# Kernel tuning notes

Hardware: AMD Instinct MI355X
Metric: run time of the kernel (lower is better)

The kernel has to match this reference:

```python
import jax, jax.numpy as jnp
import numpy as np

G, N, D_IN, H = 512, 128, 128, 256  # graphs, nodes/graph, input feat, hidden


def setup_inputs() -> dict:
    key = jax.random.key(0)
    ks = jax.random.split(key, 12)
    node_features = jax.random.normal(ks[0], (G, N, D_IN), dtype=jnp.float32)
    # sparse-ish symmetric binary adjacency with self-loops (avg degree ~ 6)
    a = (jax.random.uniform(ks[1], (G, N, N)) < 0.05).astype(jnp.float32)
    adj = jnp.clip(a + jnp.swapaxes(a, 1, 2) + jnp.eye(N, dtype=jnp.float32)[None], 0.0, 1.0)
    s = 0.02
    W1 = jax.random.normal(ks[2], (D_IN, H), dtype=jnp.float32) * s
    b1 = jnp.zeros((H,), dtype=jnp.float32)
    W2 = jax.random.normal(ks[3], (H, H), dtype=jnp.float32) * s
    b2 = jnp.zeros((H,), dtype=jnp.float32)
    W3 = jax.random.normal(ks[4], (H, H), dtype=jnp.float32) * s
    b3 = jnp.zeros((H,), dtype=jnp.float32)
    Wh = jax.random.normal(ks[5], (H, 1), dtype=jnp.float32) * s
    bh = jnp.zeros((1,), dtype=jnp.float32)
    return {"node_features": node_features, "adj": adj, "W1": W1, "b1": b1,
            "W2": W2, "b2": b2, "W3": W3, "b3": b3, "Wh": Wh, "bh": bh}


def _gcn_layer(x, adj, W, b):
    # x: [G,N,d], adj: [G,N,N] -> relu(adj @ x @ W + b)
    agg = jnp.einsum('gij,gjd->gid', adj, x)
    return jax.nn.relu(jnp.einsum('gid,dh->gih', agg, W) + b)


def reference(node_features, adj, W1, b1, W2, b2, W3, b3, Wh, bh):
    x = node_features
    # per-layer conv; dropout is identity at inference (training=False)
    x = _gcn_layer(x, adj, W1, b1)
    x = _gcn_layer(x, adj, W2, b2)
    x = _gcn_layer(x, adj, W3, b3)
    pooled = jnp.mean(x, axis=1)               # [G, H] mean readout
    yhat = pooled @ Wh + bh                    # [G, 1] linear head
    return jnp.squeeze(yhat, axis=-1)          # [G]
```

## Files before the change

### kernel.cpp

```cpp
#include <hip/hip_runtime.h>
#include <hip/hip_bf16.h>

typedef __attribute__((ext_vector_type(8))) short bf16x8;
typedef __attribute__((ext_vector_type(4))) float f32x4;

#define PX 136
#define PA 136
#define PW 72
#define PG 72

static __device__ __forceinline__ unsigned short f2b(float f) {
  union { __hip_bfloat16 h; unsigned short u; } cv;
  cv.h = __float2bfloat16(f);
  return cv.u;
}

__global__ void __launch_bounds__(256) gnn_prep(const float* __restrict__ W1,
                                                const float* __restrict__ W2,
                                                const float* __restrict__ W3,
                                                unsigned short* __restrict__ wt) {
  int idx = blockIdx.x * 256 + threadIdx.x;
  unsigned short* wt1 = wt;
  unsigned short* wt2 = wt + 32768;
  unsigned short* wt3 = wt + 98304;
  if (idx < 32768) {
    int d = idx >> 8, h = idx & 255;
    wt1[h * 128 + d] = f2b(W1[idx]);
  }
  {
    int d = idx >> 8, h = idx & 255;
    wt2[h * 256 + d] = f2b(W2[idx]);
    wt3[h * 256 + d] = f2b(W3[idx]);
  }
}

__global__ void __launch_bounds__(512, 2) gnn_main(
    const float* __restrict__ xin, const float* __restrict__ adjg,
    const float* __restrict__ b1, const float* __restrict__ b2,
    const float* __restrict__ b3, const float* __restrict__ Wh,
    const float* __restrict__ bh, const unsigned short* __restrict__ wt,
    float* __restrict__ out) {
  __shared__ unsigned short sXT[256 * PX];
  __shared__ unsigned short sAdj[128 * PA];
  __shared__ unsigned short sW[256 * PW];
  __shared__ unsigned short sAggC[128 * PG];

  const int g = blockIdx.x;
  const int tid = threadIdx.x;
  const int lane = tid & 63;
  const int w = tid >> 6;
  const int l15 = lane & 15;
  const int l4 = lane >> 4;
  const int wm = w & 1;
  const int wn = w >> 1;

  const float* x0 = xin + (size_t)g * (128 * 128);
  const float* ag = adjg + (size_t)g * (128 * 128);

  {
    int row = tid >> 2;
    int c0 = (tid & 3) << 5;
    const float4* asrc = (const float4*)(ag + row * 128 + c0);
    const float4* xsrc = (const float4*)(x0 + row * 128 + c0);
#pragma unroll
    for (int q = 0; q < 8; ++q) {
      float4 v = asrc[q];
      ushort4 p;
      p.x = f2b(v.x); p.y = f2b(v.y); p.z = f2b(v.z); p.w = f2b(v.w);
      *(ushort4*)&sAdj[row * PA + c0 + q * 4] = p;
    }
#pragma unroll
    for (int q = 0; q < 8; ++q) {
      float4 v = xsrc[q];
      int d = c0 + q * 4;
      sXT[(d + 0) * PX + row] = f2b(v.x);
      sXT[(d + 1) * PX + row] = f2b(v.y);
      sXT[(d + 2) * PX + row] = f2b(v.z);
      sXT[(d + 3) * PX + row] = f2b(v.w);
    }
  }
  __syncthreads();

  f32x4 accB[4][4];

  for (int l = 0; l < 3; ++l) {
    const int Din = (l == 0) ? 128 : 256;
    const int nck = Din >> 6;
    const unsigned short* wtl = (l == 0) ? wt : (l == 1) ? wt + 32768 : wt + 98304;
    const float* bl = (l == 0) ? b1 : (l == 1) ? b2 : b3;

#pragma unroll
    for (int mi = 0; mi < 4; ++mi)
#pragma unroll
      for (int ni = 0; ni < 4; ++ni)
        accB[mi][ni] = (f32x4){0.f, 0.f, 0.f, 0.f};

    for (int c = 0; c < nck; ++c) {
      {
        int h = tid >> 1;
        int cc = (tid & 1) << 5;
        const unsigned short* src = wtl + h * Din + (c << 6) + cc;
#pragma unroll
        for (int q = 0; q < 4; ++q) {
          bf16x8 v = *(const bf16x8*)(src + q * 8);
          *(bf16x8*)&sW[h * PW + cc + q * 8] = v;
        }
      }
      f32x4 accA[2][2];
#pragma unroll
      for (int mi = 0; mi < 2; ++mi)
#pragma unroll
        for (int ni = 0; ni < 2; ++ni)
          accA[mi][ni] = (f32x4){0.f, 0.f, 0.f, 0.f};

#pragma unroll
      for (int ks = 0; ks < 4; ++ks) {
        bf16x8 a[2], b[2];
#pragma unroll
        for (int mi = 0; mi < 2; ++mi) {
          int dr = (c << 6) + wm * 32 + mi * 16 + l15;
          a[mi] = *(const bf16x8*)&sXT[dr * PX + ks * 32 + l4 * 8];
        }
#pragma unroll
        for (int ni = 0; ni < 2; ++ni) {
          int ir = wn * 32 + ni * 16 + l15;
          b[ni] = *(const bf16x8*)&sAdj[ir * PA + ks * 32 + l4 * 8];
        }
#pragma unroll
        for (int mi = 0; mi < 2; ++mi)
#pragma unroll
          for (int ni = 0; ni < 2; ++ni)
            accA[mi][ni] = __builtin_amdgcn_mfma_f32_16x16x32_bf16(a[mi], b[ni], accA[mi][ni], 0, 0, 0);
      }
#pragma unroll
      for (int mi = 0; mi < 2; ++mi)
#pragma unroll
        for (int ni = 0; ni < 2; ++ni) {
          int dloc = wm * 32 + mi * 16 + l4 * 4;
          int i = wn * 32 + ni * 16 + l15;
          f32x4 v = accA[mi][ni];
          ushort4 p;
          p.x = f2b(v[0]); p.y = f2b(v[1]); p.z = f2b(v[2]); p.w = f2b(v[3]);
          *(ushort4*)&sAggC[i * PG + dloc] = p;
        }
      __syncthreads();
#pragma unroll
      for (int ks = 0; ks < 2; ++ks) {
        bf16x8 a[4], b[4];
#pragma unroll
        for (int mi = 0; mi < 4; ++mi) {
          int ir = wm * 64 + mi * 16 + l15;
          a[mi] = *(const bf16x8*)&sAggC[ir * PG + ks * 32 + l4 * 8];
        }
#pragma unroll
        for (int ni = 0; ni < 4; ++ni) {
          int hr = wn * 64 + ni * 16 + l15;
          b[ni] = *(const bf16x8*)&sW[hr * PW + ks * 32 + l4 * 8];
        }
#pragma unroll
        for (int mi = 0; mi < 4; ++mi)
#pragma unroll
          for (int ni = 0; ni < 4; ++ni)
            accB[mi][ni] = __builtin_amdgcn_mfma_f32_16x16x32_bf16(a[mi], b[ni], accB[mi][ni], 0, 0, 0);
      }
      __syncthreads();
    }

    float bias[4];
#pragma unroll
    for (int ni = 0; ni < 4; ++ni) bias[ni] = bl[wn * 64 + ni * 16 + l15];

    if (l < 2) {
#pragma unroll
      for (int ni = 0; ni < 4; ++ni) {
        int h = wn * 64 + ni * 16 + l15;
#pragma unroll
        for (int mi = 0; mi < 4; ++mi) {
          int i0 = wm * 64 + mi * 16 + l4 * 4;
          ushort4 p;
          p.x = f2b(fmaxf(accB[mi][ni][0] + bias[ni], 0.f));
          p.y = f2b(fmaxf(accB[mi][ni][1] + bias[ni], 0.f));
          p.z = f2b(fmaxf(accB[mi][ni][2] + bias[ni], 0.f));
          p.w = f2b(fmaxf(accB[mi][ni][3] + bias[ni], 0.f));
          *(ushort4*)&sXT[h * PX + i0] = p;
        }
      }
      __syncthreads();
    } else {
      float* sPool = (float*)sAggC;
      float ps[4];
#pragma unroll
      for (int ni = 0; ni < 4; ++ni) {
        float s = 0.f;
#pragma unroll
        for (int mi = 0; mi < 4; ++mi)
#pragma unroll
          for (int r = 0; r < 4; ++r)
            s += fmaxf(accB[mi][ni][r] + bias[ni], 0.f);
        s += __shfl_xor(s, 16);
        s += __shfl_xor(s, 32);
        ps[ni] = s;
      }
      if (l4 == 0) {
#pragma unroll
        for (int ni = 0; ni < 4; ++ni)
          sPool[wm * 256 + wn * 64 + ni * 16 + l15] = ps[ni];
      }
      __syncthreads();
      if (w == 0) {
        float acc = 0.f;
#pragma unroll
        for (int q = 0; q < 4; ++q) {
          int h = lane + q * 64;
          acc += (sPool[h] + sPool[256 + h]) * Wh[h];
        }
#pragma unroll
        for (int off = 32; off > 0; off >>= 1) acc += __shfl_xor(acc, off);
        if (lane == 0) out[g] = acc * (1.0f / 128.0f) + bh[0];
      }
    }
  }
}

extern "C" void kernel_launch(void* const* d_in, const int* in_sizes, int n_in,
                              void* d_out, int out_size, void* d_ws, size_t ws_size,
                              hipStream_t stream) {
  const float* xin = (const float*)d_in[0];
  const float* adj = (const float*)d_in[1];
  const float* W1  = (const float*)d_in[2];
  const float* b1  = (const float*)d_in[3];
  const float* W2  = (const float*)d_in[4];
  const float* b2  = (const float*)d_in[5];
  const float* W3  = (const float*)d_in[6];
  const float* b3  = (const float*)d_in[7];
  const float* Wh  = (const float*)d_in[8];
  const float* bh  = (const float*)d_in[9];
  unsigned short* wt = (unsigned short*)d_ws;

  gnn_prep<<<256, 256, 0, stream>>>(W1, W2, W3, wt);
  gnn_main<<<512, 512, 0, stream>>>(xin, adj, b1, b2, b3, Wh, bh, wt, (float*)d_out);
}
```

Baseline: 62.76 us.

## Pre-transpose x in separate kernel, keep adj and W fragments in registers, swizzle LDS

Adds a kernel that converts node features to bf16 and transposes them into workspace, so the main kernel can copy them into LDS with contiguous 16-byte loads. Adjacency fragments are loaded straight into registers and packed once, which removes the sAdj buffer. Weight fragments are read from global or L2 per chunk instead of being staged through LDS. The remaining LDS buffers use XOR swizzles instead of padding, and launch bounds now ask for 4 blocks per CU. In exchange there is an extra launch, an extra global round trip for x, and higher register pressure.

```diff
diff --git a/kernel.cpp b/kernel.cpp
--- a/kernel.cpp
+++ b/kernel.cpp
@@ -3,16 +3,18 @@
 
 typedef __attribute__((ext_vector_type(8))) short bf16x8;
 typedef __attribute__((ext_vector_type(4))) float f32x4;
-
-#define PX 136
-#define PA 136
-#define PW 72
-#define PG 72
 
 static __device__ __forceinline__ unsigned short f2b(float f) {
   union { __hip_bfloat16 h; unsigned short u; } cv;
   cv.h = __float2bfloat16(f);
   return cv.u;
+}
+
+static __device__ __forceinline__ bf16x8 pack8(float4 a, float4 b) {
+  bf16x8 r;
+  r[0] = (short)f2b(a.x); r[1] = (short)f2b(a.y); r[2] = (short)f2b(a.z); r[3] = (short)f2b(a.w);
+  r[4] = (short)f2b(b.x); r[5] = (short)f2b(b.y); r[6] = (short)f2b(b.z); r[7] = (short)f2b(b.w);
+  return r;
 }
 
 __global__ void __launch_bounds__(256) gnn_prep(const float* __restrict__ W1,
@@ -23,62 +25,83 @@
   unsigned short* wt1 = wt;
   unsigned short* wt2 = wt + 32768;
   unsigned short* wt3 = wt + 98304;
-  if (idx < 32768) {
-    int d = idx >> 8, h = idx & 255;
-    wt1[h * 128 + d] = f2b(W1[idx]);
-  }
-  {
-    int d = idx >> 8, h = idx & 255;
-    wt2[h * 256 + d] = f2b(W2[idx]);
-    wt3[h * 256 + d] = f2b(W3[idx]);
-  }
-}
-
-__global__ void __launch_bounds__(512, 2) gnn_main(
-    const float* __restrict__ xin, const float* __restrict__ adjg,
+  if (idx < 32768) { int d = idx >> 8, h = idx & 255; wt1[h * 128 + d] = f2b(W1[idx]); }
+  { int d = idx >> 8, h = idx & 255; wt2[h * 256 + d] = f2b(W2[idx]); wt3[h * 256 + d] = f2b(W3[idx]); }
+}
+
+__global__ void __launch_bounds__(256) tp_x(const float* __restrict__ xin,
+                                            unsigned short* __restrict__ xt0) {
+  __shared__ unsigned short sT[128 * 128];
+  int g = blockIdx.x, t = threadIdx.x;
+  const float* xg = xin + (size_t)g * 16384;
+#pragma unroll
+  for (int v = 0; v < 4; ++v) {
+    int bi = v * 256 + t;
+    int db = bi & 31, jb = bi >> 5;
+    int j0 = jb * 4, d0 = db * 4;
+    float4 r0 = *(const float4*)(xg + (j0 + 0) * 128 + d0);
+    float4 r1 = *(const float4*)(xg + (j0 + 1) * 128 + d0);
+    float4 r2 = *(const float4*)(xg + (j0 + 2) * 128 + d0);
+    float4 r3 = *(const float4*)(xg + (j0 + 3) * 128 + d0);
+    int coff = ((jb * 8) ^ ((db & 15) << 4)) >> 1;
+    *(ushort4*)&sT[(d0 + 0) * 128 + coff] = make_ushort4(f2b(r0.x), f2b(r1.x), f2b(r2.x), f2b(r3.x));
+    *(ushort4*)&sT[(d0 + 1) * 128 + coff] = make_ushort4(f2b(r0.y), f2b(r1.y), f2b(r2.y), f2b(r3.y));
+    *(ushort4*)&sT[(d0 + 2) * 128 + coff] = make_ushort4(f2b(r0.z), f2b(r1.z), f2b(r2.z), f2b(r3.z));
+    *(ushort4*)&sT[(d0 + 3) * 128 + coff] = make_ushort4(f2b(r0.w), f2b(r1.w), f2b(r2.w), f2b(r3.w));
+  }
+  __syncthreads();
+  unsigned short* og = xt0 + (size_t)g * 16384;
+#pragma unroll
+  for (int it = 0; it < 8; ++it) {
+    int e = it * 2048 + t * 8;
+    int d = e >> 7, j0 = e & 127;
+    int cidx = ((j0 * 2) ^ (((d >> 2) & 15) << 4)) >> 1;
+    *(bf16x8*)(og + e) = *(const bf16x8*)&sT[d * 128 + cidx];
+  }
+}
+
+#define XS(d, colb) ((d) * 128 + ((((colb)) ^ (((d) & 15) << 4)) >> 1))
+#define AGS(i, colb) ((i) * 64 + ((((colb)) ^ (((i) & 7) << 4)) >> 1))
+
+__global__ void __launch_bounds__(512, 4) gnn_main(
+    const float* __restrict__ adjg,
     const float* __restrict__ b1, const float* __restrict__ b2,
     const float* __restrict__ b3, const float* __restrict__ Wh,
-    const float* __restrict__ bh, const unsigned short* __restrict__ wt,
-    float* __restrict__ out) {
-  __shared__ unsigned short sXT[256 * PX];
-  __shared__ unsigned short sAdj[128 * PA];
-  __shared__ unsigned short sW[256 * PW];
-  __shared__ unsigned short sAggC[128 * PG];
-
-  const int g = blockIdx.x;
-  const int tid = threadIdx.x;
-  const int lane = tid & 63;
-  const int w = tid >> 6;
-  const int l15 = lane & 15;
-  const int l4 = lane >> 4;
-  const int wm = w & 1;
-  const int wn = w >> 1;
-
-  const float* x0 = xin + (size_t)g * (128 * 128);
-  const float* ag = adjg + (size_t)g * (128 * 128);
-
-  {
-    int row = tid >> 2;
-    int c0 = (tid & 3) << 5;
-    const float4* asrc = (const float4*)(ag + row * 128 + c0);
-    const float4* xsrc = (const float4*)(x0 + row * 128 + c0);
-#pragma unroll
-    for (int q = 0; q < 8; ++q) {
-      float4 v = asrc[q];
-      ushort4 p;
-      p.x = f2b(v.x); p.y = f2b(v.y); p.z = f2b(v.z); p.w = f2b(v.w);
-      *(ushort4*)&sAdj[row * PA + c0 + q * 4] = p;
+    const float* __restrict__ bh, const unsigned short* __restrict__ xt0,
+    const unsigned short* __restrict__ wt, float* __restrict__ out) {
+  __shared__ unsigned short sXT[256 * 128];
+  __shared__ unsigned short sAggC[128 * 64];
+
+  const int g = blockIdx.x, tid = threadIdx.x;
+  const int lane = tid & 63, w = tid >> 6;
+  const int l15 = lane & 15, l4 = lane >> 4;
+  const int wm = w & 1, wn = w >> 1;
+
+  const float* ag = adjg + (size_t)g * 16384;
+  const unsigned short* xg = xt0 + (size_t)g * 16384;
+
+  float4 araw[2][4][2];
+#pragma unroll
+  for (int ni = 0; ni < 2; ++ni) {
+    int ir = wn * 32 + ni * 16 + l15;
+#pragma unroll
+    for (int ks = 0; ks < 4; ++ks) {
+      araw[ni][ks][0] = *(const float4*)(ag + ir * 128 + ks * 32 + l4 * 8);
+      araw[ni][ks][1] = *(const float4*)(ag + ir * 128 + ks * 32 + l4 * 8 + 4);
     }
-#pragma unroll
-    for (int q = 0; q < 8; ++q) {
-      float4 v = xsrc[q];
-      int d = c0 + q * 4;
-      sXT[(d + 0) * PX + row] = f2b(v.x);
-      sXT[(d + 1) * PX + row] = f2b(v.y);
-      sXT[(d + 2) * PX + row] = f2b(v.z);
-      sXT[(d + 3) * PX + row] = f2b(v.w);
-    }
-  }
+  }
+#pragma unroll
+  for (int it = 0; it < 4; ++it) {
+    int off = it * 8192 + tid * 16;
+    int row = off >> 8, colb = off & 255;
+    *(bf16x8*)&sXT[XS(row, colb)] = *(const bf16x8*)(xg + (off >> 1));
+  }
+  bf16x8 adjF[2][4];
+#pragma unroll
+  for (int ni = 0; ni < 2; ++ni)
+#pragma unroll
+    for (int ks = 0; ks < 4; ++ks)
+      adjF[ni][ks] = pack8(araw[ni][ks][0], araw[ni][ks][1]);
   __syncthreads();
 
   f32x4 accB[4][4];
@@ -88,50 +111,43 @@
     const int nck = Din >> 6;
     const unsigned short* wtl = (l == 0) ? wt : (l == 1) ? wt + 32768 : wt + 98304;
     const float* bl = (l == 0) ? b1 : (l == 1) ? b2 : b3;
+    float bias[4];
+#pragma unroll
+    for (int ni = 0; ni < 4; ++ni) bias[ni] = bl[wn * 64 + ni * 16 + l15];
 
 #pragma unroll
     for (int mi = 0; mi < 4; ++mi)
 #pragma unroll
-      for (int ni = 0; ni < 4; ++ni)
-        accB[mi][ni] = (f32x4){0.f, 0.f, 0.f, 0.f};
+      for (int ni = 0; ni < 4; ++ni) accB[mi][ni] = (f32x4){0.f, 0.f, 0.f, 0.f};
 
     for (int c = 0; c < nck; ++c) {
-      {
-        int h = tid >> 1;
-        int cc = (tid & 1) << 5;
-        const unsigned short* src = wtl + h * Din + (c << 6) + cc;
-#pragma unroll
-        for (int q = 0; q < 4; ++q) {
-          bf16x8 v = *(const bf16x8*)(src + q * 8);
-          *(bf16x8*)&sW[h * PW + cc + q * 8] = v;
-        }
-      }
       f32x4 accA[2][2];
 #pragma unroll
       for (int mi = 0; mi < 2; ++mi)
 #pragma unroll
-        for (int ni = 0; ni < 2; ++ni)
-          accA[mi][ni] = (f32x4){0.f, 0.f, 0.f, 0.f};
-
+        for (int ni = 0; ni < 2; ++ni) accA[mi][ni] = (f32x4){0.f, 0.f, 0.f, 0.f};
 #pragma unroll
       for (int ks = 0; ks < 4; ++ks) {
-        bf16x8 a[2], b[2];
+        bf16x8 a[2];
 #pragma unroll
         for (int mi = 0; mi < 2; ++mi) {
-          int dr = (c << 6) + wm * 32 + mi * 16 + l15;
-          a[mi] = *(const bf16x8*)&sXT[dr * PX + ks * 32 + l4 * 8];
-        }
-#pragma unroll
-        for (int ni = 0; ni < 2; ++ni) {
-          int ir = wn * 32 + ni * 16 + l15;
-          b[ni] = *(const bf16x8*)&sAdj[ir * PA + ks * 32 + l4 * 8];
+          int dr = c * 64 + wm * 32 + mi * 16 + l15;
+          a[mi] = *(const bf16x8*)&sXT[XS(dr, ks * 64 + l4 * 16)];
         }
 #pragma unroll
         for (int mi = 0; mi < 2; ++mi)
 #pragma unroll
           for (int ni = 0; ni < 2; ++ni)
-            accA[mi][ni] = __builtin_amdgcn_mfma_f32_16x16x32_bf16(a[mi], b[ni], accA[mi][ni], 0, 0, 0);
-      }
+            accA[mi][ni] = __builtin_amdgcn_mfma_f32_16x16x32_bf16(a[mi], adjF[ni][ks], accA[mi][ni], 0, 0, 0);
+      }
+      bf16x8 wf[2][4];
+#pragma unroll
+      for (int ks = 0; ks < 2; ++ks)
+#pragma unroll
+        for (int ni = 0; ni < 4; ++ni) {
+          int hr = wn * 64 + ni * 16 + l15;
+          wf[ks][ni] = *(const bf16x8*)(wtl + hr * Din + c * 64 + ks * 32 + l4 * 8);
+        }
 #pragma unroll
       for (int mi = 0; mi < 2; ++mi)
 #pragma unroll
@@ -139,36 +155,26 @@
           int dloc = wm * 32 + mi * 16 + l4 * 4;
           int i = wn * 32 + ni * 16 + l15;
           f32x4 v = accA[mi][ni];
-          ushort4 p;
-          p.x = f2b(v[0]); p.y = f2b(v[1]); p.z = f2b(v[2]); p.w = f2b(v[3]);
-          *(ushort4*)&sAggC[i * PG + dloc] = p;
+          *(ushort4*)&sAggC[AGS(i, 2 * dloc)] =
+              make_ushort4(f2b(v[0]), f2b(v[1]), f2b(v[2]), f2b(v[3]));
         }
       __syncthreads();
 #pragma unroll
       for (int ks = 0; ks < 2; ++ks) {
-        bf16x8 a[4], b[4];
+        bf16x8 a[4];
 #pragma unroll
         for (int mi = 0; mi < 4; ++mi) {
           int ir = wm * 64 + mi * 16 + l15;
-          a[mi] = *(const bf16x8*)&sAggC[ir * PG + ks * 32 + l4 * 8];
-        }
-#pragma unroll
-        for (int ni = 0; ni < 4; ++ni) {
-          int hr = wn * 64 + ni * 16 + l15;
-          b[ni] = *(const bf16x8*)&sW[hr * PW + ks * 32 + l4 * 8];
+          a[mi] = *(const bf16x8*)&sAggC[AGS(ir, ks * 64 + l4 * 16)];
         }
 #pragma unroll
         for (int mi = 0; mi < 4; ++mi)
 #pragma unroll
           for (int ni = 0; ni < 4; ++ni)
-            accB[mi][ni] = __builtin_amdgcn_mfma_f32_16x16x32_bf16(a[mi], b[ni], accB[mi][ni], 0, 0, 0);
+            accB[mi][ni] = __builtin_amdgcn_mfma_f32_16x16x32_bf16(a[mi], wf[ks][ni], accB[mi][ni], 0, 0, 0);
       }
       __syncthreads();
     }
-
-    float bias[4];
-#pragma unroll
-    for (int ni = 0; ni < 4; ++ni) bias[ni] = bl[wn * 64 + ni * 16 + l15];
 
     if (l < 2) {
 #pragma unroll
@@ -177,12 +183,10 @@
 #pragma unroll
         for (int mi = 0; mi < 4; ++mi) {
           int i0 = wm * 64 + mi * 16 + l4 * 4;
-          ushort4 p;
-          p.x = f2b(fmaxf(accB[mi][ni][0] + bias[ni], 0.f));
-          p.y = f2b(fmaxf(accB[mi][ni][1] + bias[ni], 0.f));
-          p.z = f2b(fmaxf(accB[mi][ni][2] + bias[ni], 0.f));
-          p.w = f2b(fmaxf(accB[mi][ni][3] + bias[ni], 0.f));
-          *(ushort4*)&sXT[h * PX + i0] = p;
+          f32x4 v = accB[mi][ni];
+          *(ushort4*)&sXT[XS(h, 2 * i0)] = make_ushort4(
+              f2b(fmaxf(v[0] + bias[ni], 0.f)), f2b(fmaxf(v[1] + bias[ni], 0.f)),
+              f2b(fmaxf(v[2] + bias[ni], 0.f)), f2b(fmaxf(v[3] + bias[ni], 0.f)));
         }
       }
       __syncthreads();
@@ -195,16 +199,14 @@
 #pragma unroll
         for (int mi = 0; mi < 4; ++mi)
 #pragma unroll
-          for (int r = 0; r < 4; ++r)
-            s += fmaxf(accB[mi][ni][r] + bias[ni], 0.f);
+          for (int r = 0; r < 4; ++r) s += fmaxf(accB[mi][ni][r] + bias[ni], 0.f);
         s += __shfl_xor(s, 16);
         s += __shfl_xor(s, 32);
         ps[ni] = s;
       }
       if (l4 == 0) {
 #pragma unroll
-        for (int ni = 0; ni < 4; ++ni)
-          sPool[wm * 256 + wn * 64 + ni * 16 + l15] = ps[ni];
+        for (int ni = 0; ni < 4; ++ni) sPool[wm * 256 + wn * 64 + ni * 16 + l15] = ps[ni];
       }
       __syncthreads();
       if (w == 0) {
@@ -235,8 +237,11 @@
   const float* b3  = (const float*)d_in[7];
   const float* Wh  = (const float*)d_in[8];
   const float* bh  = (const float*)d_in[9];
-  unsigned short* wt = (unsigned short*)d_ws;
-
+
+  unsigned short* xt0 = (unsigned short*)d_ws;
+  unsigned short* wt  = xt0 + (size_t)512 * 16384;
+
+  tp_x<<<512, 256, 0, stream>>>(xin, xt0);
   gnn_prep<<<256, 256, 0, stream>>>(W1, W2, W3, wt);
-  gnn_main<<<512, 512, 0, stream>>>(xin, adj, b1, b2, b3, Wh, bh, wt, (float*)d_out);
-}
+  gnn_main<<<512, 512, 0, stream>>>(adj, b1, b2, b3, Wh, bh, xt0, wt, (float*)d_out);
+}
```

New measurement: 116.0 us. 84.8% more time.
